# Kernel tuning notes

Hardware: AMD Instinct MI355X
Metric: run time of the kernel (lower is better)

The kernel has to match this reference:

```python
import jax, jax.numpy as jnp
import numpy as np

B, T, C = 1, 2048, 2048
H, G, D = 16, 4, 128   # n_head, n_query_groups, head_size
I = 8192               # intermediate_size


def _hv(x, alpha, beta):
    # ParamHeaveside forward: alpha * heaviside(x - beta)
    return (alpha * (x - beta > 0).astype(x.dtype)).astype(x.dtype)


def _normed_linear(x, w, scale):
    # NormedLinear: column-center then L2-normalize columns (dim=0), scaled
    w = w - w.mean(axis=0, keepdims=True)
    n = jnp.maximum(jnp.sqrt((w * w).sum(axis=0, keepdims=True)), 1e-12)
    return x @ (scale * w / n).T


def _rope(t, cos, sin):
    # non-interleaved rotary (rotate-half), cos/sin: [T, D/2]
    half = t.shape[-1] // 2
    t1, t2 = t[..., :half], t[..., half:]
    c, s = cos[None, :, None, :], sin[None, :, None, :]
    return jnp.concatenate([t1 * c - t2 * s, t1 * s + t2 * c], axis=-1)


def _block(x, cos, sin, attn_w, proj_w, proj_scale, fc_w, mlp_proj_w, mlp_proj_scale,
           in_alpha, in_beta, q_alpha, q_beta, k_alpha, k_beta,
           out_alpha, out_beta, act1_alpha, act1_beta, act2_alpha, act2_beta, hv):
    q_per_kv = H // G
    h = hv(x, in_alpha, in_beta)                      # encoder_input (norm is identity)
    qkv = (h @ attn_w.T).reshape(B, T, G, q_per_kv + 2, D)
    q = qkv[:, :, :, :q_per_kv, :].reshape(B, T, H, D)
    k = qkv[:, :, :, q_per_kv, :]                     # [B,T,G,D]
    v = qkv[:, :, :, q_per_kv + 1, :]                 # [B,T,G,D]
    q = hv(_rope(q, cos, sin), q_alpha, q_beta)
    k = hv(_rope(k, cos, sin), k_alpha, k_beta)
    q = q.transpose(0, 2, 1, 3)                       # [B,H,T,D]
    k = jnp.repeat(k.transpose(0, 2, 1, 3), q_per_kv, axis=1)
    v = jnp.repeat(v.transpose(0, 2, 1, 3), q_per_kv, axis=1)
    scores = jnp.einsum('bhtd,bhsd->bhts', q, k) * (1.0 / D)  # scale = 1/head_size
    causal = jnp.tril(jnp.ones((T, T), bool))
    w = jnp.where(causal[None, None], jax.nn.relu(scores), 0.0)  # relu-attention
    y = jnp.einsum('bhts,bhsd->bhtd', w, v).transpose(0, 2, 1, 3).reshape(B, T, C)
    y = _normed_linear(hv(y, out_alpha, out_beta), proj_w, proj_scale)
    x = x + y
    m = hv(x, act1_alpha, act1_beta) @ fc_w.T
    m = _normed_linear(hv(m, act2_alpha, act2_beta), mlp_proj_w, mlp_proj_scale)
    return x + m


def setup_inputs() -> dict:
    key = jax.random.key(0)
    ks = jax.random.split(key, 8)
    rn = lambda k, s, sc=0.02: (jax.random.normal(k, s) * sc).astype(jnp.float32)
    theta = 1.0 / (10000.0 ** (jnp.arange(0, D, 2, dtype=jnp.float32) / D))
    idx = jnp.outer(jnp.arange(T, dtype=jnp.float32), theta)
    return {
        'x': jax.random.normal(ks[0], (B, T, C), dtype=jnp.float32),
        'cos': jnp.cos(idx), 'sin': jnp.sin(idx),
        'attn_w': rn(ks[1], ((H + 2 * G) * D, C)),
        'proj_w': rn(ks[2], (C, C)), 'proj_scale': jnp.float32(0.01),
        'fc_w': rn(ks[3], (I, C)),
        'mlp_proj_w': rn(ks[4], (C, I)), 'mlp_proj_scale': jnp.float32(0.01),
        'in_alpha': jnp.full((C,), 0.5, jnp.float32), 'in_beta': rn(ks[5], (C,), 0.01),
        'q_alpha': jnp.full((D,), 0.5, jnp.float32), 'q_beta': jnp.zeros((D,), jnp.float32),
        'k_alpha': jnp.full((D,), 0.5, jnp.float32), 'k_beta': jnp.zeros((D,), jnp.float32),
        'out_alpha': jnp.full((C,), 0.5, jnp.float32), 'out_beta': rn(ks[6], (C,), 0.01),
        'act1_alpha': jnp.full((C,), 0.5, jnp.float32), 'act1_beta': rn(ks[7], (C,), 0.01),
        'act2_alpha': jnp.full((I,), 0.5, jnp.float32), 'act2_beta': jnp.zeros((I,), jnp.float32),
    }


def reference(x, cos, sin, attn_w, proj_w, proj_scale, fc_w, mlp_proj_w, mlp_proj_scale,
              in_alpha, in_beta, q_alpha, q_beta, k_alpha, k_beta,
              out_alpha, out_beta, act1_alpha, act1_beta, act2_alpha, act2_beta):
    return _block(x, cos, sin, attn_w, proj_w, proj_scale, fc_w, mlp_proj_w, mlp_proj_scale,
                  in_alpha, in_beta, q_alpha, q_beta, k_alpha, k_beta,
                  out_alpha, out_beta, act1_alpha, act1_beta, act2_alpha, act2_beta, _hv)
```

## Files before the change

kernel.cpp:

```cpp
#include <hip/hip_runtime.h>

typedef __attribute__((ext_vector_type(8))) short short8;
typedef __attribute__((ext_vector_type(4))) float f32x4;
typedef __attribute__((ext_vector_type(4))) int i32x4;

constexpr int TT = 2048, CC = 2048, HQ = 16, GG = 4, DD = 128, IC = 8192;

__device__ __forceinline__ ushort f2b(float f) {
  union { float f; unsigned u; } v; v.f = f;
  unsigned r = v.u + 0x7fffu + ((v.u >> 16) & 1u);
  return (ushort)(r >> 16);
}
__device__ __forceinline__ float b2f(ushort u) {
  union { unsigned u; float f; } v; v.u = ((unsigned)u) << 16; return v.f;
}
__device__ __forceinline__ char q8(float eff, float r) {
  float q = rintf(eff * r);
  q = fminf(fmaxf(q, -127.f), 127.f);
  return (char)(int)q;
}

__device__ __forceinline__ void gload16(const void* g, void* l) {
  __builtin_amdgcn_global_load_lds(
      (const __attribute__((address_space(1))) void*)g,
      (__attribute__((address_space(3))) void*)l, 16, 0, 0);
}

#define BAR()    __builtin_amdgcn_s_barrier()
#define PRIO1()  __builtin_amdgcn_s_setprio(1)
#define PRIO0()  __builtin_amdgcn_s_setprio(0)

template<int EPI>
__global__ __launch_bounds__(512, 2)
void gemm_i8(const char* __restrict__ A, const char* __restrict__ B,
             void* __restrict__ C0, const float* __restrict__ s,
             const float* __restrict__ beta, int M, int N, int K, int kc)
{
  __shared__ alignas(16) char lds[131072];
  const int tid = threadIdx.x;
  const int l = tid & 63, w = tid >> 6;
  const int fl = l & 15, fh = l >> 4;
  const int wrm = w >> 2, wcn = w & 3;
  const int m0 = blockIdx.y * 256, n0 = blockIdx.x * 256;
  const int kBeg = blockIdx.z * kc;
  const int kEnd = (kBeg + kc < K) ? kBeg + kc : K;
  const int nt = (kEnd - kBeg) >> 7;

  i32x4 acc[8][4] = {};

  const int srow = tid >> 3;
  const int scol = ((tid & 7) ^ (srow & 7)) * 16;
  const char* Ag = A + (size_t)(m0 + srow) * K + kBeg + scol;
  const char* Bg = B + (size_t)(n0 + srow) * K + kBeg + scol;

  auto stage_half = [&](int tile, int h) {
    const char* base = (h < 2) ? Ag : Bg;
    const int half = h & 1;
    const char* g = base + (size_t)(half * 128) * K + tile * 128;
    char* d = lds + (tile & 1) * 65536 + ((h < 2) ? 0 : 32768) + half * 16384 + tid * 16;
    gload16(g, d);
    gload16(g + (size_t)64 * K, d + 8192);
  };

  auto readA = [&](i32x4 (&dst)[4][2], int buf, int mofs) {
#pragma unroll
    for (int mf = 0; mf < 4; ++mf)
#pragma unroll
      for (int ks = 0; ks < 2; ++ks) {
        int row = wrm * 128 + (mofs + mf) * 16 + fl;
        dst[mf][ks] = *(const i32x4*)(lds + buf * 65536 + row * 128 +
                                      (((ks * 4 + fh) ^ (row & 7)) * 16));
      }
  };
  auto readB = [&](i32x4 (&dst)[2][2], int buf, int nofs) {
#pragma unroll
    for (int nf = 0; nf < 2; ++nf)
#pragma unroll
      for (int ks = 0; ks < 2; ++ks) {
        int row = wcn * 64 + (nofs + nf) * 16 + fl;
        dst[nf][ks] = *(const i32x4*)(lds + buf * 65536 + 32768 + row * 128 +
                                      (((ks * 4 + fh) ^ (row & 7)) * 16));
      }
  };
  auto mmQ = [&](i32x4 (&a)[4][2], i32x4 (&b)[2][2], int mo, int no) {
    PRIO1();
#pragma unroll
    for (int mf = 0; mf < 4; ++mf)
#pragma unroll
      for (int nf = 0; nf < 2; ++nf)
#pragma unroll
        for (int ks = 0; ks < 2; ++ks)
          acc[mo + mf][no + nf] = __builtin_amdgcn_mfma_i32_16x16x64_i8(
              a[mf][ks], b[nf][ks], acc[mo + mf][no + nf], 0, 0, 0);
    PRIO0();
  };

  stage_half(0, 0); stage_half(0, 1); stage_half(0, 2); stage_half(0, 3);
  if (nt > 1) {
    stage_half(1, 2); stage_half(1, 3);
    asm volatile("s_waitcnt vmcnt(4)" ::: "memory");
  } else {
    asm volatile("s_waitcnt vmcnt(0)" ::: "memory");
  }
  BAR();

  for (int t = 0; t < nt; ++t) {
    const int buf = t & 1;
    i32x4 A0[4][2], A1[4][2], B0[2][2], B1[2][2];

    readA(A0, buf, 0);
    readB(B0, buf, 0);
    if (t + 1 < nt) stage_half(t + 1, 0);
    BAR();
    mmQ(A0, B0, 0, 0);

    readB(B1, buf, 2);
    if (t + 1 < nt) stage_half(t + 1, 1);
    BAR();
    mmQ(A0, B1, 0, 2);

    readA(A1, buf, 4);
    BAR();
    mmQ(A1, B0, 4, 0);

    if (t + 2 < nt) { stage_half(t + 2, 2); stage_half(t + 2, 3); }
    if (t <= nt - 3) asm volatile("s_waitcnt vmcnt(4)" ::: "memory");
    else             asm volatile("s_waitcnt vmcnt(0)" ::: "memory");
    BAR();
    mmQ(A1, B1, 4, 2);
  }

  const int orow0 = m0 + wrm * 128 + fh * 4;
  const int ocol0 = n0 + wcn * 64 + fl;
#pragma unroll
  for (int mf = 0; mf < 8; ++mf) {
#pragma unroll
    for (int nf = 0; nf < 4; ++nf) {
      const int c = ocol0 + nf * 16;
      const float sc = s[c];
#pragma unroll
      for (int j = 0; j < 4; ++j) {
        const int r = orow0 + mf * 16 + j;
        const size_t o = (size_t)r * N + c;
        float v = (float)acc[mf][nf][j] * sc;
        if constexpr (EPI == 1) {
          ((char*)C0)[o] = (v - beta[c] > 0.f) ? (char)1 : (char)0;
        } else {
          ((ushort*)C0 + (size_t)blockIdx.z * M * N)[o] = f2b(v);
        }
      }
    }
  }
}

template<int NS, int MODE>
__global__ void reduce_kernel(const ushort* p0, const ushort* p1, const ushort* p2, const ushort* p3,
                              const float* resid, float* outf, char* outb,
                              const float* beta, int n4, int cols)
{
  const ushort* ps[4] = {p0, p1, p2, p3};
  for (int i = blockIdx.x * blockDim.x + threadIdx.x; i < n4; i += gridDim.x * blockDim.x) {
    float4 s = ((const float4*)resid)[i];
#pragma unroll
    for (int z = 0; z < NS; ++z) {
      ushort4 q = ((const ushort4*)ps[z])[i];
      s.x += b2f(q.x); s.y += b2f(q.y); s.z += b2f(q.z); s.w += b2f(q.w);
    }
    ((float4*)outf)[i] = s;
    if constexpr (MODE == 1) {
      int c = (i * 4) & (cols - 1);
      char4 r;
      r.x = (s.x - beta[c] > 0.f) ? 1 : 0;
      r.y = (s.y - beta[c + 1] > 0.f) ? 1 : 0;
      r.z = (s.z - beta[c + 2] > 0.f) ? 1 : 0;
      r.w = (s.w - beta[c + 3] > 0.f) ? 1 : 0;
      ((char4*)outb)[i] = r;
    }
  }
}

__global__ __launch_bounds__(256)
void attn_kernel(const ushort* __restrict__ qb, const ushort* __restrict__ kb,
                 const ushort* __restrict__ vt, char* __restrict__ hy,
                 const float* __restrict__ obeta)
{
  __shared__ alignas(16) ushort Qs[64 * 128];
  __shared__ alignas(16) ushort Ks[64 * 128];
  __shared__ alignas(16) ushort Vs[128 * 64];
  __shared__ alignas(16) ushort Ps[64 * 64];
  const int bx = blockIdx.x;
  const int h = blockIdx.y;
  const int qi = (h & 8) ? bx : (31 - bx);
  const int g = h >> 2;
  const int q0 = qi * 64;
  const int tid = threadIdx.x;
  const int w = tid >> 6, l = tid & 63;
  const int fl = l & 15, fh = l >> 4;

#pragma unroll
  for (int i = 0; i < 4; ++i) {
    int row = w * 16 + i * 4 + (l >> 4);
    int c16 = (l & 15) ^ (row & 7);
    gload16(qb + (size_t)h * TT * DD + (size_t)(q0 + row) * DD + c16 * 8,
            (char*)Qs + (w << 12) + (i << 10) + (l << 4));
  }

  f32x4 oacc[8] = {};

  for (int s0 = 0; s0 <= q0; s0 += 64) {
#pragma unroll
    for (int i = 0; i < 4; ++i) {
      int row = w * 16 + i * 4 + (l >> 4);
      int c16 = (l & 15) ^ (row & 7);
      gload16(kb + (size_t)g * TT * DD + (size_t)(s0 + row) * DD + c16 * 8,
              (char*)Ks + (w << 12) + (i << 10) + (l << 4));
    }
#pragma unroll
    for (int i = 0; i < 4; ++i) {
      int d = w * 32 + i * 8 + (l >> 3);
      int c16 = (l & 7) ^ (d & 7);
      gload16(vt + (size_t)g * DD * TT + (size_t)d * TT + s0 + c16 * 8,
              (char*)Vs + (w << 12) + (i << 10) + (l << 4));
    }
    __syncthreads();

    f32x4 sacc[4] = {};
    const int qrow = w * 16 + fl;
#pragma unroll
    for (int ks = 0; ks < 4; ++ks) {
      int slotA = (ks * 4 + fh) ^ (qrow & 7);
      short8 a = *(const short8*)((char*)Qs + qrow * 256 + slotA * 16);
#pragma unroll
      for (int n = 0; n < 4; ++n) {
        int krow = n * 16 + fl;
        int slotB = (ks * 4 + fh) ^ (krow & 7);
        short8 b = *(const short8*)((char*)Ks + krow * 256 + slotB * 16);
        sacc[n] = __builtin_amdgcn_mfma_f32_16x16x32_bf16(a, b, sacc[n], 0, 0, 0);
      }
    }

#pragma unroll
    for (int n = 0; n < 4; ++n) {
      const int scol = s0 + n * 16 + fl;
#pragma unroll
      for (int j = 0; j < 4; ++j) {
        const int pr = w * 16 + fh * 4 + j;
        const int qr = q0 + pr;
        float v = sacc[n][j] * 0.0078125f;
        ushort pv = (scol <= qr && v > 0.f) ? f2b(v) : (ushort)0;
        int slot = ((n * 2) + (fl >> 3)) ^ (pr & 7);
        ((ushort*)((char*)Ps + pr * 128 + slot * 16))[fl & 7] = pv;
      }
    }

    const int prow = w * 16 + fl;
#pragma unroll
    for (int ks = 0; ks < 2; ++ks) {
      int slotA = (ks * 4 + fh) ^ (prow & 7);
      short8 pa = *(const short8*)((char*)Ps + prow * 128 + slotA * 16);
#pragma unroll
      for (int n = 0; n < 8; ++n) {
        int vrow = n * 16 + fl;
        int slotB = (ks * 4 + fh) ^ (vrow & 7);
        short8 vb = *(const short8*)((char*)Vs + vrow * 128 + slotB * 16);
        oacc[n] = __builtin_amdgcn_mfma_f32_16x16x32_bf16(pa, vb, oacc[n], 0, 0, 0);
      }
    }
    __syncthreads();
  }

#pragma unroll
  for (int n = 0; n < 8; ++n) {
    const int c = h * DD + n * 16 + fl;
    const float be = obeta[c];
#pragma unroll
    for (int j = 0; j < 4; ++j) {
      const int tq = q0 + w * 16 + fh * 4 + j;
      float v = oacc[n][j];
      hy[(size_t)tq * CC + c] = (v - be > 0.f) ? (char)1 : (char)0;
    }
  }
}

__global__ __launch_bounds__(256)
void rope_hv_kernel(const ushort* __restrict__ qp0, const ushort* __restrict__ qp1,
                    const float* __restrict__ cs, const float* __restrict__ sn,
                    const float* __restrict__ qalpha, const float* __restrict__ qbeta,
                    const float* __restrict__ kalpha, const float* __restrict__ kbeta,
                    ushort* __restrict__ qb, ushort* __restrict__ kb,
                    ushort* __restrict__ vt)
{
  __shared__ ushort Vsh[64][129];
  const int t0 = blockIdx.x * 64, g = blockIdx.y, job = blockIdx.z;
  const int tid = threadIdx.x;
  if (job < 5) {
    const int hh = job;
    const float* alpha = (hh < 4) ? qalpha : kalpha;
    const float* beta = (hh < 4) ? qbeta : kbeta;
    const int hoff = (hh < 4) ? hh * 128 : 512;
    for (int it = 0; it < 16; ++it) {
      int idx = it * 256 + tid;
      int tr = idx >> 6, dd = idx & 63;
      size_t base = (size_t)(t0 + tr) * 3072 + g * 768 + hoff;
      float x1 = b2f(qp0[base + dd]) + b2f(qp1[base + dd]);
      float x2 = b2f(qp0[base + 64 + dd]) + b2f(qp1[base + 64 + dd]);
      float c = cs[(size_t)(t0 + tr) * 64 + dd];
      float s = sn[(size_t)(t0 + tr) * 64 + dd];
      float o1 = x1 * c - x2 * s, o2 = x1 * s + x2 * c;
      ushort b1 = (o1 - beta[dd] > 0.f) ? f2b(alpha[dd]) : (ushort)0;
      ushort b2 = (o2 - beta[64 + dd] > 0.f) ? f2b(alpha[64 + dd]) : (ushort)0;
      if (hh < 4) {
        size_t o = ((size_t)(g * 4 + hh) * TT + t0 + tr) * DD;
        qb[o + dd] = b1;
        qb[o + 64 + dd] = b2;
      } else {
        size_t o = ((size_t)g * TT + t0 + tr) * DD;
        kb[o + dd] = b1;
        kb[o + 64 + dd] = b2;
      }
    }
  } else {
    for (int it = 0; it < 32; ++it) {
      int idx = it * 256 + tid;
      int tr = idx >> 7, d = idx & 127;
      size_t src = (size_t)(t0 + tr) * 3072 + g * 768 + 640 + d;
      Vsh[tr][d] = f2b(b2f(qp0[src]) + b2f(qp1[src]));
    }
    __syncthreads();
    for (int it = 0; it < 32; ++it) {
      int idx = it * 256 + tid;
      int d = idx >> 6, tl = idx & 63;
      vt[((size_t)g * DD + d) * TT + t0 + tl] = Vsh[tl][d];
    }
  }
}

__global__ __launch_bounds__(256)
void quant_fused(const float* __restrict__ attn_w, char* __restrict__ attn_q,
                 const float* __restrict__ fc_w, char* __restrict__ fc_q,
                 const float* __restrict__ proj_w, char* __restrict__ proj_q,
                 const float* __restrict__ mlp_w, char* __restrict__ mlp_q,
                 const float* __restrict__ inA, const float* __restrict__ a1A,
                 const float* __restrict__ pmu, const float* __restrict__ pinv,
                 const float* __restrict__ outA,
                 const float* __restrict__ mmu, const float* __restrict__ minv,
                 const float* __restrict__ a2A,
                 float* __restrict__ s_all,
                 const float* __restrict__ x, const float* __restrict__ ib,
                 char* __restrict__ h_in)
{
  __shared__ float wmax[4];
  const int bx = blockIdx.x;
  const int tid = threadIdx.x;
  const int wv = tid >> 6, lane = tid & 63;

  if (bx < 3328) {
    const float* W; char* Q; const float4* A4;
    const float4* MU4 = nullptr; const float4* INV4 = nullptr;
    int row, sofs;
    if (bx < 768)       { W = attn_w; Q = attn_q; A4 = (const float4*)inA;  row = bx * 4 + wv;          sofs = 0; }
    else if (bx < 2816) { W = fc_w;   Q = fc_q;   A4 = (const float4*)a1A;  row = (bx - 768) * 4 + wv;  sofs = 3072; }
    else                { W = proj_w; Q = proj_q; A4 = (const float4*)outA; row = (bx - 2816) * 4 + wv; sofs = 11264;
                          MU4 = (const float4*)pmu; INV4 = (const float4*)pinv; }
    const float4* src = (const float4*)(W + (size_t)row * 2048);
    char4* dst = (char4*)(Q + (size_t)row * 2048);
    float4 ef[8];
    float m = 0.f;
#pragma unroll
    for (int it = 0; it < 8; ++it) {
      int i = it * 64 + lane;
      float4 v = src[i];
      float4 a = A4[i];
      float4 e;
      if (MU4) {
        float4 mu = MU4[i], iv = INV4[i];
        e.x = (v.x - mu.x) * iv.x * a.x;
        e.y = (v.y - mu.y) * iv.y * a.y;
        e.z = (v.z - mu.z) * iv.z * a.z;
        e.w = (v.w - mu.w) * iv.w * a.w;
      } else {
        e.x = v.x * a.x; e.y = v.y * a.y; e.z = v.z * a.z; e.w = v.w * a.w;
      }
      ef[it] = e;
      m = fmaxf(m, fmaxf(fmaxf(fabsf(e.x), fabsf(e.y)), fmaxf(fabsf(e.z), fabsf(e.w))));
    }
    for (int mask = 32; mask; mask >>= 1) m = fmaxf(m, __shfl_xor(m, mask));
    if (lane == 0) s_all[sofs + row] = m * (1.f / 127.f);
    const float r = (m > 0.f) ? 127.f / m : 0.f;
#pragma unroll
    for (int it = 0; it < 8; ++it) {
      int i = it * 64 + lane;
      char4 q;
      q.x = q8(ef[it].x, r); q.y = q8(ef[it].y, r);
      q.z = q8(ef[it].z, r); q.w = q8(ef[it].w, r);
      dst[i] = q;
    }
  } else if (bx < 5376) {
    const int row = bx - 3328;
    const float4* src = (const float4*)(mlp_w + (size_t)row * 8192);
    const float4* MU4 = (const float4*)mmu;
    const float4* INV4 = (const float4*)minv;
    const float4* A4 = (const float4*)a2A;
    char4* dst = (char4*)(mlp_q + (size_t)row * 8192);
    float4 ef[8];
    float m = 0.f;
#pragma unroll
    for (int it = 0; it < 8; ++it) {
      int i = wv * 512 + it * 64 + lane;
      float4 v = src[i];
      float4 mu = MU4[i], iv = INV4[i], a = A4[i];
      float4 e;
      e.x = (v.x - mu.x) * iv.x * a.x;
      e.y = (v.y - mu.y) * iv.y * a.y;
      e.z = (v.z - mu.z) * iv.z * a.z;
      e.w = (v.w - mu.w) * iv.w * a.w;
      ef[it] = e;
      m = fmaxf(m, fmaxf(fmaxf(fabsf(e.x), fabsf(e.y)), fmaxf(fabsf(e.z), fabsf(e.w))));
    }
    for (int mask = 32; mask; mask >>= 1) m = fmaxf(m, __shfl_xor(m, mask));
    if (lane == 0) wmax[wv] = m;
    __syncthreads();
    m = fmaxf(fmaxf(wmax[0], wmax[1]), fmaxf(wmax[2], wmax[3]));
    if (tid == 0) s_all[13312 + row] = m * (1.f / 127.f);
    const float r = (m > 0.f) ? 127.f / m : 0.f;
#pragma unroll
    for (int it = 0; it < 8; ++it) {
      int i = wv * 512 + it * 64 + lane;
      char4 q;
      q.x = q8(ef[it].x, r); q.y = q8(ef[it].y, r);
      q.z = q8(ef[it].z, r); q.w = q8(ef[it].w, r);
      dst[i] = q;
    }
  } else {
    const int blk = bx - 5376;
    const int stride = 512 * 256;
    const float4* ib4 = (const float4*)ib;
    for (int i = blk * 256 + tid; i < 2048 * 2048 / 4; i += stride) {
      float4 v = ((const float4*)x)[i];
      float4 b = ib4[i & 511];
      char4 q;
      q.x = (v.x - b.x > 0.f) ? 1 : 0;
      q.y = (v.y - b.y > 0.f) ? 1 : 0;
      q.z = (v.z - b.z > 0.f) ? 1 : 0;
      q.w = (v.w - b.w > 0.f) ? 1 : 0;
      ((char4*)h_in)[i] = q;
    }
  }
}

__global__ void stats1_all(const float* __restrict__ pw, const float* __restrict__ mw,
                           float* __restrict__ ps, float* __restrict__ ps2,
                           float* __restrict__ ms, float* __restrict__ ms2)
{
  const int bx = blockIdx.x, chunk = blockIdx.y;
  const float* W;
  float* os; float* os2; int cols, j;
  if (bx < 8) { W = pw; os = ps; os2 = ps2; cols = 2048; j = bx * 256 + threadIdx.x; }
  else        { W = mw; os = ms; os2 = ms2; cols = 8192; j = (bx - 8) * 256 + threadIdx.x; }
  const float* p = W + (size_t)chunk * 128 * cols + j;
  float s = 0.f, s2 = 0.f;
  for (int i = 0; i < 128; ++i) { float v = p[(size_t)i * cols]; s += v; s2 += v * v; }
  os[chunk * cols + j] = s;
  os2[chunk * cols + j] = s2;
}

__global__ void stats2_all(const float* __restrict__ ps, const float* __restrict__ ps2,
                           float* __restrict__ p_mu, float* __restrict__ p_inv,
                           const float* __restrict__ pscale,
                           const float* __restrict__ ms, const float* __restrict__ ms2,
                           float* __restrict__ m_mu, float* __restrict__ m_inv,
                           const float* __restrict__ mscale)
{
  const int bx = blockIdx.x;
  const float* S; const float* S2; float* mu; float* inv; const float* sc; int cols, j;
  if (bx < 8) { S = ps; S2 = ps2; mu = p_mu; inv = p_inv; sc = pscale; cols = 2048; j = bx * 256 + threadIdx.x; }
  else        { S = ms; S2 = ms2; mu = m_mu; inv = m_inv; sc = mscale; cols = 8192; j = (bx - 8) * 256 + threadIdx.x; }
  float s = 0.f, s2 = 0.f;
  for (int c = 0; c < 16; ++c) { s += S[c * cols + j]; s2 += S2[c * cols + j]; }
  float m = s * (1.f / 2048.f);
  float var = s2 - s * m;
  float nn = sqrtf(fmaxf(var, 0.f));
  nn = fmaxf(nn, 1e-12f);
  mu[j] = m;
  inv[j] = sc[0] / nn;
}

extern "C" void kernel_launch(void* const* d_in, const int* in_sizes, int n_in,
                              void* d_out, int out_size, void* d_ws, size_t ws_size,
                              hipStream_t stream) {
  const float* x          = (const float*)d_in[0];
  const float* cosT       = (const float*)d_in[1];
  const float* sinT       = (const float*)d_in[2];
  const float* attn_w     = (const float*)d_in[3];
  const float* proj_w     = (const float*)d_in[4];
  const float* proj_scale = (const float*)d_in[5];
  const float* fc_w       = (const float*)d_in[6];
  const float* mlp_proj_w = (const float*)d_in[7];
  const float* mlp_scale  = (const float*)d_in[8];
  const float* in_alpha   = (const float*)d_in[9];
  const float* in_beta    = (const float*)d_in[10];
  const float* q_alpha    = (const float*)d_in[11];
  const float* q_beta     = (const float*)d_in[12];
  const float* k_alpha    = (const float*)d_in[13];
  const float* k_beta     = (const float*)d_in[14];
  const float* out_alpha  = (const float*)d_in[15];
  const float* out_beta   = (const float*)d_in[16];
  const float* act1_alpha = (const float*)d_in[17];
  const float* act1_beta  = (const float*)d_in[18];
  const float* act2_alpha = (const float*)d_in[19];
  const float* act2_beta  = (const float*)d_in[20];

  char* cur = (char*)d_ws;
  auto alloc = [&](size_t b) { void* p = cur; cur += (b + 255) & ~(size_t)255; return p; };

  char* attn_q = (char*)alloc((size_t)3072 * 2048);
  char* fc_q   = (char*)alloc((size_t)8192 * 2048);
  char* proj_q = (char*)alloc((size_t)2048 * 2048);
  char* mlp_q  = (char*)alloc((size_t)2048 * 8192);
  char* h_in   = (char*)alloc((size_t)2048 * 2048);
  char* h_y    = (char*)alloc((size_t)2048 * 2048);
  char* h2     = (char*)alloc((size_t)2048 * 2048);
  char* h3     = (char*)alloc((size_t)2048 * 8192);
  ushort* qbuf  = (ushort*)alloc((size_t)HQ * TT * DD * 2);
  ushort* kbuf  = (ushort*)alloc((size_t)GG * TT * DD * 2);
  ushort* vtbuf = (ushort*)alloc((size_t)GG * DD * TT * 2);
  float* x2 = (float*)alloc((size_t)2048 * 2048 * 4);
  ushort* qkv_parts  = (ushort*)alloc((size_t)2 * 2048 * 3072 * 2);
  ushort* proj_parts = (ushort*)alloc((size_t)4 * 2048 * 2048 * 2);
  ushort* mlp_parts  = (ushort*)alloc((size_t)4 * 2048 * 2048 * 2);
  float* pp_s  = (float*)alloc(16 * 2048 * 4);
  float* pp_s2 = (float*)alloc(16 * 2048 * 4);
  float* mp_s  = (float*)alloc(16 * 8192 * 4);
  float* mp_s2 = (float*)alloc(16 * 8192 * 4);
  float* p_mu  = (float*)alloc(2048 * 4);
  float* p_inv = (float*)alloc(2048 * 4);
  float* m_mu  = (float*)alloc(8192 * 4);
  float* m_inv = (float*)alloc(8192 * 4);
  float* s_all = (float*)alloc(15360 * 4);

  const size_t PLANE_QKV = (size_t)2048 * 3072;
  const size_t PLANE     = (size_t)2048 * 2048;

  float* s_attn = s_all;
  float* s_fc   = s_all + 3072;
  float* s_proj = s_all + 11264;
  float* s_mlp  = s_all + 13312;

  stats1_all<<<dim3(40, 16), 256, 0, stream>>>(proj_w, mlp_proj_w, pp_s, pp_s2, mp_s, mp_s2);
  stats2_all<<<40, 256, 0, stream>>>(pp_s, pp_s2, p_mu, p_inv, proj_scale,
                                     mp_s, mp_s2, m_mu, m_inv, mlp_scale);
  quant_fused<<<5888, 256, 0, stream>>>(attn_w, attn_q, fc_w, fc_q, proj_w, proj_q,
                                        mlp_proj_w, mlp_q,
                                        in_alpha, act1_alpha, p_mu, p_inv, out_alpha,
                                        m_mu, m_inv, act2_alpha, s_all,
                                        x, in_beta, h_in);

  gemm_i8<3><<<dim3(3072 / 256, 2048 / 256, 2), 512, 0, stream>>>(
      h_in, attn_q, qkv_parts, s_attn, nullptr, 2048, 3072, 2048, 1024);

  rope_hv_kernel<<<dim3(TT / 64, GG, 6), 256, 0, stream>>>(
      qkv_parts, qkv_parts + PLANE_QKV, cosT, sinT,
      q_alpha, q_beta, k_alpha, k_beta, qbuf, kbuf, vtbuf);

  attn_kernel<<<dim3(TT / 64, HQ), 256, 0, stream>>>(qbuf, kbuf, vtbuf, h_y, out_beta);

  gemm_i8<3><<<dim3(2048 / 256, 2048 / 256, 4), 512, 0, stream>>>(
      h_y, proj_q, proj_parts, s_proj, nullptr, 2048, 2048, 2048, 512);
  reduce_kernel<4, 1><<<2048, 256, 0, stream>>>(
      proj_parts, proj_parts + PLANE, proj_parts + 2 * PLANE, proj_parts + 3 * PLANE,
      x, x2, h2, act1_beta, 2048 * 2048 / 4, 2048);

  gemm_i8<1><<<dim3(8192 / 256, 2048 / 256, 1), 512, 0, stream>>>(
      h2, fc_q, h3, s_fc, act2_beta, 2048, 8192, 2048, 2048);

  gemm_i8<3><<<dim3(8, 8, 4), 512, 0, stream>>>(
      h3, mlp_q, mlp_parts, s_mlp, nullptr, 2048, 2048, 8192, 2048);
  reduce_kernel<4, 2><<<2048, 256, 0, stream>>>(
      mlp_parts, mlp_parts + PLANE, mlp_parts + 2 * PLANE, mlp_parts + 3 * PLANE,
      x2, (float*)d_out, nullptr, nullptr, 2048 * 2048 / 4, 1);
}
```

Before: 274.0 us.

## Double-buffer K/V tiles in attention and hold Q fragments in registers

The attention kernel now keeps two LDS buffers for the K and V tiles and prefetches the next key block while the current one is being computed. Before, the kernel loaded a tile and then synchronised, so each tile load was exposed. The Q fragments are now loaded straight from global memory into registers once, which drops the Q LDS tile and the repeated LDS reads of Q. In exchange the kernel uses more LDS and more registers, which may lower occupancy.

```diff
diff --git a/kernel.cpp b/kernel.cpp
--- a/kernel.cpp
+++ b/kernel.cpp
@@ -184,9 +184,8 @@
                  const ushort* __restrict__ vt, char* __restrict__ hy,
                  const float* __restrict__ obeta)
 {
-  __shared__ alignas(16) ushort Qs[64 * 128];
-  __shared__ alignas(16) ushort Ks[64 * 128];
-  __shared__ alignas(16) ushort Vs[128 * 64];
+  __shared__ alignas(16) ushort Ks[2][64 * 128];
+  __shared__ alignas(16) ushort Vs[2][128 * 64];
   __shared__ alignas(16) ushort Ps[64 * 64];
   const int bx = blockIdx.x;
   const int h = blockIdx.y;
@@ -197,45 +196,52 @@
   const int w = tid >> 6, l = tid & 63;
   const int fl = l & 15, fh = l >> 4;
 
-#pragma unroll
-  for (int i = 0; i < 4; ++i) {
-    int row = w * 16 + i * 4 + (l >> 4);
-    int c16 = (l & 15) ^ (row & 7);
-    gload16(qb + (size_t)h * TT * DD + (size_t)(q0 + row) * DD + c16 * 8,
-            (char*)Qs + (w << 12) + (i << 10) + (l << 4));
-  }
-
-  f32x4 oacc[8] = {};
-
-  for (int s0 = 0; s0 <= q0; s0 += 64) {
+  auto stageK = [&](int buf, int s0t) {
 #pragma unroll
     for (int i = 0; i < 4; ++i) {
       int row = w * 16 + i * 4 + (l >> 4);
       int c16 = (l & 15) ^ (row & 7);
-      gload16(kb + (size_t)g * TT * DD + (size_t)(s0 + row) * DD + c16 * 8,
-              (char*)Ks + (w << 12) + (i << 10) + (l << 4));
-    }
+      gload16(kb + (size_t)g * TT * DD + (size_t)(s0t + row) * DD + c16 * 8,
+              (char*)Ks[buf] + (w << 12) + (i << 10) + (l << 4));
+    }
+  };
+  auto stageV = [&](int buf, int s0t) {
 #pragma unroll
     for (int i = 0; i < 4; ++i) {
       int d = w * 32 + i * 8 + (l >> 3);
       int c16 = (l & 7) ^ (d & 7);
-      gload16(vt + (size_t)g * DD * TT + (size_t)d * TT + s0 + c16 * 8,
-              (char*)Vs + (w << 12) + (i << 10) + (l << 4));
-    }
-    __syncthreads();
+      gload16(vt + (size_t)g * DD * TT + (size_t)d * TT + s0t + c16 * 8,
+              (char*)Vs[buf] + (w << 12) + (i << 10) + (l << 4));
+    }
+  };
+
+  short8 qf[4];
+  {
+    const ushort* qp = qb + (size_t)h * TT * DD + (size_t)(q0 + w * 16 + fl) * DD + fh * 8;
+#pragma unroll
+    for (int ks = 0; ks < 4; ++ks) qf[ks] = *(const short8*)(qp + ks * 32);
+  }
+
+  stageK(0, 0); stageV(0, 0);
+  asm volatile("s_waitcnt vmcnt(0)" ::: "memory");
+  BAR();
+
+  f32x4 oacc[8] = {};
+  int buf = 0;
+
+  for (int s0 = 0; s0 <= q0; s0 += 64) {
+    const bool more = (s0 + 64 <= q0);
+    if (more) { stageK(buf ^ 1, s0 + 64); stageV(buf ^ 1, s0 + 64); }
 
     f32x4 sacc[4] = {};
-    const int qrow = w * 16 + fl;
 #pragma unroll
     for (int ks = 0; ks < 4; ++ks) {
-      int slotA = (ks * 4 + fh) ^ (qrow & 7);
-      short8 a = *(const short8*)((char*)Qs + qrow * 256 + slotA * 16);
 #pragma unroll
       for (int n = 0; n < 4; ++n) {
         int krow = n * 16 + fl;
         int slotB = (ks * 4 + fh) ^ (krow & 7);
-        short8 b = *(const short8*)((char*)Ks + krow * 256 + slotB * 16);
-        sacc[n] = __builtin_amdgcn_mfma_f32_16x16x32_bf16(a, b, sacc[n], 0, 0, 0);
+        short8 b = *(const short8*)((char*)Ks[buf] + krow * 256 + slotB * 16);
+        sacc[n] = __builtin_amdgcn_mfma_f32_16x16x32_bf16(qf[ks], b, sacc[n], 0, 0, 0);
       }
     }
 
@@ -262,11 +268,16 @@
       for (int n = 0; n < 8; ++n) {
         int vrow = n * 16 + fl;
         int slotB = (ks * 4 + fh) ^ (vrow & 7);
-        short8 vb = *(const short8*)((char*)Vs + vrow * 128 + slotB * 16);
+        short8 vb = *(const short8*)((char*)Vs[buf] + vrow * 128 + slotB * 16);
         oacc[n] = __builtin_amdgcn_mfma_f32_16x16x32_bf16(pa, vb, oacc[n], 0, 0, 0);
       }
     }
-    __syncthreads();
+
+    if (more) {
+      asm volatile("s_waitcnt vmcnt(0)" ::: "memory");
+      BAR();
+      buf ^= 1;
+    }
   }
 
 #pragma unroll
```

Result: no change. 274.4 us (+0.1%).
